# Performance work log

Measured on AMD Instinct MI355X. Metric: run time of the kernel, lower is better.

The kernel has to match this reference:

```python
import jax, jax.numpy as jnp
import numpy as np

N = 50000
E = 800000
HIDDEN = 128
NUM_HEADS = 8
D_HEAD = HIDDEN // NUM_HEADS


def setup_inputs() -> dict:
    key = jax.random.key(0)
    ks = jax.random.split(key, 12)
    sc = 1.0 / np.sqrt(HIDDEN)
    inp = {
        "h": jax.random.normal(ks[0], (N, HIDDEN), dtype=jnp.float32),
        "rows": jax.random.randint(ks[1], (E,), 0, N, dtype=jnp.int32),
        "cols": jax.random.randint(ks[2], (E,), 0, N, dtype=jnp.int32),
        "Wq": jax.random.normal(ks[3], (HIDDEN, HIDDEN), dtype=jnp.float32) * sc,
        "bq": jax.random.normal(ks[4], (HIDDEN,), dtype=jnp.float32) * sc,
        "Wk": jax.random.normal(ks[5], (HIDDEN, HIDDEN), dtype=jnp.float32) * sc,
        "bk": jax.random.normal(ks[6], (HIDDEN,), dtype=jnp.float32) * sc,
        "Wv": jax.random.normal(ks[7], (HIDDEN, HIDDEN), dtype=jnp.float32) * sc,
        "bv": jax.random.normal(ks[8], (HIDDEN,), dtype=jnp.float32) * sc,
        "Wo": jax.random.normal(ks[9], (HIDDEN, HIDDEN), dtype=jnp.float32) * sc,
        "bo": jax.random.normal(ks[10], (HIDDEN,), dtype=jnp.float32) * sc,
    }
    return inp


def reference(h, rows, cols, Wq, bq, Wk, bk, Wv, bv, Wo, bo):
    n = h.shape[0]
    scaling = D_HEAD ** (-0.5)
    # projections; torch-style reshape splits hidden as (d_head, num_heads)
    q = ((h @ Wq.T + bq).reshape(n, D_HEAD, NUM_HEADS)) * scaling
    k = (h @ Wk.T + bk).reshape(n, D_HEAD, NUM_HEADS)
    v = (h @ Wv.T + bv).reshape(n, D_HEAD, NUM_HEADS)
    # SDDMM: per-edge, per-head score = q[row] . k[col]   -> [E, H]
    scores = jnp.einsum("edh,edh->eh", q[rows], k[cols])
    # row-wise (destination) stable softmax over variable-degree neighborhoods
    m = jax.ops.segment_max(scores, rows, num_segments=n)  # [N, H]
    e = jnp.exp(scores - m[rows])
    s = jax.ops.segment_sum(e, rows, num_segments=n)  # [N, H]
    attn = e / s[rows]  # [E, H]
    # SpMM: out[i] = sum_{(i,j) in E} attn[e] * v[j]
    out = jax.ops.segment_sum(attn[:, None, :] * v[cols], rows, num_segments=n)
    return out.reshape(n, HIDDEN) @ Wo.T + bo
```

## Files before the change

kernel.cpp:

```cpp
#include <hip/hip_runtime.h>
#include <math.h>

#define N_NODES 50000
#define N_EDGES 800000
#define HID 128
#define CAP 64

#define SCAT_TH   (N_EDGES / 8)
#define SCAT_BLK  ((SCAT_TH + 255) / 256)
#define WCVT_BLK  64
#define HCVT_BLK  (N_NODES * HID / 4 / 256)
#define PREP_BLK  (SCAT_BLK + WCVT_BLK + HCVT_BLK)

#define QKV_BX    ((N_NODES + 31) / 32)
#define ATTN_BLK  ((N_NODES + 3) / 4)
#define OUT_BLK   ((N_NODES + 63) / 64)

typedef _Float16 f16_t;
typedef f16_t f16x8 __attribute__((ext_vector_type(8)));
typedef f16_t f16x2 __attribute__((ext_vector_type(2)));
typedef float f32x4 __attribute__((ext_vector_type(4)));

__device__ __forceinline__ ushort f2h_bits(float x) {
    union { f16_t h; ushort u; } c; c.h = (f16_t)x; return c.u;
}
__device__ __forceinline__ f16x2 as_h2(uint u) {
    union { uint u_; f16x2 h; } c; c.u_ = u; return c.h;
}

__global__ __launch_bounds__(256) void prep(
    const float* __restrict__ h,
    const float* __restrict__ Wq, const float* __restrict__ Wk,
    const float* __restrict__ Wv, const float* __restrict__ Wo,
    ushort* __restrict__ hf, ushort* __restrict__ wf,
    const int* __restrict__ rows, const int* __restrict__ cols,
    int* __restrict__ cnt, ushort* __restrict__ slots)
{
    const int b = blockIdx.x;
    const int tid = threadIdx.x;

    if (b < SCAT_BLK) {
        const int t = b * 256 + tid;
        if (t < SCAT_TH) {
            const int4* r4 = (const int4*)rows + (size_t)t * 2;
            const int4* c4 = (const int4*)cols + (size_t)t * 2;
            int4 ra = r4[0], rb2 = r4[1];
            int4 ca = c4[0], cb = c4[1];
            const int r[8] = {ra.x, ra.y, ra.z, ra.w, rb2.x, rb2.y, rb2.z, rb2.w};
            const int c[8] = {ca.x, ca.y, ca.z, ca.w, cb.x, cb.y, cb.z, cb.w};
            int p[8];
#pragma unroll
            for (int u = 0; u < 8; ++u)
                p[u] = atomicAdd(&cnt[r[u] << 4], 1);
#pragma unroll
            for (int u = 0; u < 8; ++u)
                if (p[u] < CAP) slots[(size_t)r[u] * CAP + p[u]] = (ushort)c[u];
        }
    } else if (b < SCAT_BLK + WCVT_BLK) {
        const int t = (b - SCAT_BLK) * 256 + tid;
        const int m = t >> 12, i = t & 4095;
        const float* src = (m == 0) ? Wq : (m == 1) ? Wk : (m == 2) ? Wv : Wo;
        float4 f = ((const float4*)src)[i];
        if (m < 3) {
            ushort4 o;
            o.x = f2h_bits(f.x); o.y = f2h_bits(f.y);
            o.z = f2h_bits(f.z); o.w = f2h_bits(f.w);
            ((ushort4*)(wf + m * 16384))[i] = o;
        } else {
            const int c  = i >> 5;
            const int k0 = (i & 31) * 4;
            const int d  = k0 >> 3;
            ushort* wo = wf + 3 * 16384 + c * HID + d;
            wo[((k0 + 0) & 7) << 4] = f2h_bits(f.x);
            wo[((k0 + 1) & 7) << 4] = f2h_bits(f.y);
            wo[((k0 + 2) & 7) << 4] = f2h_bits(f.z);
            wo[((k0 + 3) & 7) << 4] = f2h_bits(f.w);
        }
    } else {
        const int t = (b - SCAT_BLK - WCVT_BLK) * 256 + tid;
        float4 f = ((const float4*)h)[t];
        ushort4 o;
        o.x = f2h_bits(f.x); o.y = f2h_bits(f.y);
        o.z = f2h_bits(f.z); o.w = f2h_bits(f.w);
        ((ushort4*)hf)[t] = o;
    }
}

__global__ __launch_bounds__(256) void gemm_qkv(
    const ushort* __restrict__ hf, const ushort* __restrict__ wf,
    const float* __restrict__ bq, const float* __restrict__ bk,
    const float* __restrict__ bv,
    uint* __restrict__ qp, uint2* __restrict__ kv)
{
    const int lane = threadIdx.x & 63;
    const int wid  = threadIdx.x >> 6;
    const int mrow = lane & 15;
    const int quad = lane >> 4;
    const int rb   = blockIdx.x * 32;
    const int T    = blockIdx.y * 4 + wid;
    const int c    = ((mrow & 7) << 4) + ((mrow >> 3) << 3) + T;

    f16x8 a[2][4];
#pragma unroll
    for (int s = 0; s < 2; ++s) {
        int ar = rb + s * 16 + mrow;
        if (ar >= N_NODES) ar = N_NODES - 1;
        const ushort* ap = hf + (size_t)ar * HID + quad * 8;
#pragma unroll
        for (int kc = 0; kc < 4; ++kc) a[s][kc] = *(const f16x8*)(ap + kc * 32);
    }
    f16x8 bQ[4], bK[4], bV[4];
#pragma unroll
    for (int kc = 0; kc < 4; ++kc) {
        const int off = c * HID + kc * 32 + quad * 8;
        bQ[kc] = *(const f16x8*)(wf + off);
        bK[kc] = *(const f16x8*)(wf + 16384 + off);
        bV[kc] = *(const f16x8*)(wf + 32768 + off);
    }

    f32x4 aq[2], ak[2], av[2];
#pragma unroll
    for (int s = 0; s < 2; ++s) {
        aq[s] = (f32x4){0.f, 0.f, 0.f, 0.f};
        ak[s] = (f32x4){0.f, 0.f, 0.f, 0.f};
        av[s] = (f32x4){0.f, 0.f, 0.f, 0.f};
    }
#pragma unroll
    for (int s = 0; s < 2; ++s)
#pragma unroll
        for (int kc = 0; kc < 4; ++kc) {
            aq[s] = __builtin_amdgcn_mfma_f32_16x16x32_f16(a[s][kc], bQ[kc], aq[s], 0, 0, 0);
            ak[s] = __builtin_amdgcn_mfma_f32_16x16x32_f16(a[s][kc], bK[kc], ak[s], 0, 0, 0);
            av[s] = __builtin_amdgcn_mfma_f32_16x16x32_f16(a[s][kc], bV[kc], av[s], 0, 0, 0);
        }

    const float bqc = bq[c], bkc = bk[c], bvc = bv[c];
    const bool  lo  = (mrow & 8) == 0;
    const int   i   = mrow & 7;
#pragma unroll
    for (int s = 0; s < 2; ++s)
#pragma unroll
        for (int r = 0; r < 4; ++r) {
            const int orow = rb + s * 16 + quad * 4 + r;
            uint qv = f2h_bits((aq[s][r] + bqc) * 0.25f);
            uint kb = f2h_bits(ak[s][r] + bkc);
            uint vb = f2h_bits(av[s][r] + bvc);
            uint qh = __shfl_xor((int)qv, 8);
            uint kh = __shfl_xor((int)kb, 8);
            uint vh = __shfl_xor((int)vb, 8);
            if (lo && orow < N_NODES) {
                const size_t base = (size_t)orow * 64 + 8 * T + i;
                qp[base] = qv | (qh << 16);
                kv[base] = make_uint2(kb | (kh << 16), vb | (vh << 16));
            }
        }
}

__device__ __forceinline__ void pair_acc(uint4 rr, uint2 qu,
                                         float& l, float* O)
{
    float p = __builtin_amdgcn_fdot2(as_h2(rr.x), as_h2(qu.x), 0.f, false);
    p = __builtin_amdgcn_fdot2(as_h2(rr.z), as_h2(qu.y), p, false);
    p += __shfl_xor(p, 1);
    p += __shfl_xor(p, 2);
    const float ex = __expf(p);
    l += ex;
    const f16x2 va = as_h2(rr.y), vb = as_h2(rr.w);
    O[0] += ex * (float)va[0];
    O[1] += ex * (float)va[1];
    O[2] += ex * (float)vb[0];
    O[3] += ex * (float)vb[1];
}

__device__ __forceinline__ void pair_acc_m(uint4 rr, uint2 qu, bool ok,
                                           float& l, float* O)
{
    float p = __builtin_amdgcn_fdot2(as_h2(rr.x), as_h2(qu.x), 0.f, false);
    p = __builtin_amdgcn_fdot2(as_h2(rr.z), as_h2(qu.y), p, false);
    p += __shfl_xor(p, 1);
    p += __shfl_xor(p, 2);
    const float ex = ok ? __expf(p) : 0.f;
    l += ex;
    const f16x2 va = as_h2(rr.y), vb = as_h2(rr.w);
    O[0] += ex * (float)va[0];
    O[1] += ex * (float)va[1];
    O[2] += ex * (float)vb[0];
    O[3] += ex * (float)vb[1];
}

__global__ __launch_bounds__(256) void attn(
    const uint* __restrict__ qp, const uint2* __restrict__ kv,
    const int* __restrict__ cnt, const ushort* __restrict__ slots,
    ushort* __restrict__ ao)
{
    const int lane = threadIdx.x & 63;
    const int node = blockIdx.x * 4 + (threadIdx.x >> 6);
    if (node >= N_NODES) return;
    const int half = lane >> 5;
    const int t    = lane & 31;

    const uint2 qu = *(const uint2*)(qp + (size_t)node * 64 + 2 * t);

    int deg = cnt[node << 4];
    if (deg > CAP) deg = CAP;
    const int myslot = (lane < deg) ? (int)slots[(size_t)node * CAP + lane] : 0;

    float l0 = 0.f, l1 = 0.f, l2 = 0.f, l3 = 0.f;
    float O0[4] = {0,0,0,0}, O1[4] = {0,0,0,0};
    float O2[4] = {0,0,0,0}, O3[4] = {0,0,0,0};

    const uint4* base = (const uint4*)kv;

    int j = 0;
    for (; j + 8 <= deg; j += 8) {
        const int s0 = __shfl(myslot, j + half);
        const int s1 = __shfl(myslot, j + 2 + half);
        const int s2 = __shfl(myslot, j + 4 + half);
        const int s3 = __shfl(myslot, j + 6 + half);
        const uint4 r0 = base[(size_t)s0 * 32 + t];
        const uint4 r1 = base[(size_t)s1 * 32 + t];
        const uint4 r2 = base[(size_t)s2 * 32 + t];
        const uint4 r3 = base[(size_t)s3 * 32 + t];
        pair_acc(r0, qu, l0, O0);
        pair_acc(r1, qu, l1, O1);
        pair_acc(r2, qu, l2, O2);
        pair_acc(r3, qu, l3, O3);
    }
    for (; j < deg; j += 2) {
        const int e = j + half;
        const int s = __shfl(myslot, e);
        const uint4 rr = base[(size_t)s * 32 + t];
        pair_acc_m(rr, qu, e < deg, l0, O0);
    }

    float l = (l0 + l1) + (l2 + l3);
    float Of[4];
    Of[0] = (O0[0] + O1[0]) + (O2[0] + O3[0]);
    Of[1] = (O0[1] + O1[1]) + (O2[1] + O3[1]);
    Of[2] = (O0[2] + O1[2]) + (O2[2] + O3[2]);
    Of[3] = (O0[3] + O1[3]) + (O2[3] + O3[3]);

    l += __shfl_xor(l, 32);
    Of[0] += __shfl_xor(Of[0], 32);
    Of[1] += __shfl_xor(Of[1], 32);
    Of[2] += __shfl_xor(Of[2], 32);
    Of[3] += __shfl_xor(Of[3], 32);

    const float inv = (l > 0.f) ? 1.f / l : 0.f;

    if (half == 0) {
        ushort4 st;
        st.x = f2h_bits(Of[0] * inv);
        st.y = f2h_bits(Of[1] * inv);
        st.z = f2h_bits(Of[2] * inv);
        st.w = f2h_bits(Of[3] * inv);
        *(ushort4*)(ao + (size_t)node * HID + 4 * t) = st;
    }
}

__global__ __launch_bounds__(256) void gemm_out(
    const ushort* __restrict__ A, const ushort* __restrict__ wfo,
    const float* __restrict__ bias, float* __restrict__ out)
{
    const int lane = threadIdx.x & 63;
    const int wid  = threadIdx.x >> 6;
    const int mrow = lane & 15;
    const int quad = lane >> 4;
    const int rb   = blockIdx.x * 64;

    const int c0 = wid * 32 + mrow;
    const int c1 = c0 + 16;

    f16x8 a[4][4];
#pragma unroll
    for (int s = 0; s < 4; ++s) {
        int ar = rb + s * 16 + mrow;
        if (ar >= N_NODES) ar = N_NODES - 1;
        const ushort* ap = A + (size_t)ar * HID + quad * 8;
#pragma unroll
        for (int kc = 0; kc < 4; ++kc) a[s][kc] = *(const f16x8*)(ap + kc * 32);
    }
    f16x8 b0[4], b1[4];
#pragma unroll
    for (int kc = 0; kc < 4; ++kc) {
        b0[kc] = *(const f16x8*)(wfo + c0 * HID + kc * 32 + quad * 8);
        b1[kc] = *(const f16x8*)(wfo + c1 * HID + kc * 32 + quad * 8);
    }

    f32x4 acc[4][2];
#pragma unroll
    for (int s = 0; s < 4; ++s) {
        acc[s][0] = (f32x4){0.f, 0.f, 0.f, 0.f};
        acc[s][1] = (f32x4){0.f, 0.f, 0.f, 0.f};
    }
#pragma unroll
    for (int s = 0; s < 4; ++s)
#pragma unroll
        for (int kc = 0; kc < 4; ++kc) {
            acc[s][0] = __builtin_amdgcn_mfma_f32_16x16x32_f16(a[s][kc], b0[kc], acc[s][0], 0, 0, 0);
            acc[s][1] = __builtin_amdgcn_mfma_f32_16x16x32_f16(a[s][kc], b1[kc], acc[s][1], 0, 0, 0);
        }

    const float bc0 = bias[c0], bc1 = bias[c1];
#pragma unroll
    for (int s = 0; s < 4; ++s)
#pragma unroll
        for (int r = 0; r < 4; ++r) {
            const int orow = rb + s * 16 + quad * 4 + r;
            if (orow < N_NODES) {
                out[(size_t)orow * HID + c0] = acc[s][0][r] + bc0;
                out[(size_t)orow * HID + c1] = acc[s][1][r] + bc1;
            }
        }
}

extern "C" void kernel_launch(void* const* d_in, const int* in_sizes, int n_in,
                              void* d_out, int out_size, void* d_ws, size_t ws_size,
                              hipStream_t stream)
{
    const float* h    = (const float*)d_in[0];
    const int*   rows = (const int*)  d_in[1];
    const int*   cols = (const int*)  d_in[2];
    const float* Wq   = (const float*)d_in[3];
    const float* bq   = (const float*)d_in[4];
    const float* Wk   = (const float*)d_in[5];
    const float* bk   = (const float*)d_in[6];
    const float* Wv   = (const float*)d_in[7];
    const float* bv   = (const float*)d_in[8];
    const float* Wo   = (const float*)d_in[9];
    const float* bo   = (const float*)d_in[10];
    float* out = (float*)d_out;

    char* ws = (char*)d_ws;
    uint*   qp    = (uint*)ws;    ws += (size_t)N_NODES * 64 * 4;
    uint2*  kv    = (uint2*)ws;   ws += (size_t)N_NODES * 64 * 8;
    ushort* hf    = (ushort*)ws;  ws += (size_t)N_NODES * HID * 2;
    ushort* ao    = (ushort*)ws;  ws += (size_t)N_NODES * HID * 2;
    ushort* wf    = (ushort*)ws;  ws += 4 * 16384 * 2;
    int*    cnt   = (int*)ws;     ws += (size_t)N_NODES * 64;
    ushort* slots = (ushort*)ws;

    hipMemsetAsync(cnt, 0, (size_t)N_NODES * 64, stream);

    dim3 blk(256);
    prep<<<PREP_BLK, blk, 0, stream>>>(h, Wq, Wk, Wv, Wo, hf, wf,
                                       rows, cols, cnt, slots);
    gemm_qkv<<<dim3(QKV_BX, 2), blk, 0, stream>>>(hf, wf, bq, bk, bv, qp, kv);
    attn<<<ATTN_BLK, blk, 0, stream>>>(qp, kv, cnt, slots, ao);
    gemm_out<<<OUT_BLK, blk, 0, stream>>>(ao, wf + 3 * 16384, bo, out);
}
```

Before: 238.4 us.

## Fuse fp32-to-fp16 conversion and edge scatter into the QKV GEMM launch

Removes the separate prep pass that converted h and Wq/Wk/Wv to fp16. The QKV GEMM blocks now read fp32 h and weights directly and convert in registers. The edge scatter and Wo conversion blocks share the same launch. This drops the hf round trip through memory (a write and a re-read of N×128 halves) and one kernel launch, at the cost of reading fp32 inputs, which doubles the bytes for the A operand, and converting the weights redundantly in every block.

```diff
diff --git a/kernel.cpp b/kernel.cpp
--- a/kernel.cpp
+++ b/kernel.cpp
@@ -8,11 +8,11 @@
 
 #define SCAT_TH   (N_EDGES / 8)
 #define SCAT_BLK  ((SCAT_TH + 255) / 256)
-#define WCVT_BLK  64
-#define HCVT_BLK  (N_NODES * HID / 4 / 256)
-#define PREP_BLK  (SCAT_BLK + WCVT_BLK + HCVT_BLK)
-
+#define WOCVT_BLK 16
 #define QKV_BX    ((N_NODES + 31) / 32)
+#define QKV_BLKS  (QKV_BX * 2)
+#define FUSED1_BLK (SCAT_BLK + WOCVT_BLK + QKV_BLKS)
+
 #define ATTN_BLK  ((N_NODES + 3) / 4)
 #define OUT_BLK   ((N_NODES + 63) / 64)
 
@@ -27,14 +27,25 @@
 __device__ __forceinline__ f16x2 as_h2(uint u) {
     union { uint u_; f16x2 h; } c; c.u_ = u; return c.h;
 }
-
-__global__ __launch_bounds__(256) void prep(
+__device__ __forceinline__ f16x8 ldcvt8(const float* __restrict__ p) {
+    float4 f0 = *(const float4*)p;
+    float4 f1 = *(const float4*)(p + 4);
+    f16x8 r;
+    r[0] = (f16_t)f0.x; r[1] = (f16_t)f0.y; r[2] = (f16_t)f0.z; r[3] = (f16_t)f0.w;
+    r[4] = (f16_t)f1.x; r[5] = (f16_t)f1.y; r[6] = (f16_t)f1.z; r[7] = (f16_t)f1.w;
+    return r;
+}
+
+__global__ __launch_bounds__(256) void fused1(
     const float* __restrict__ h,
     const float* __restrict__ Wq, const float* __restrict__ Wk,
     const float* __restrict__ Wv, const float* __restrict__ Wo,
-    ushort* __restrict__ hf, ushort* __restrict__ wf,
+    const float* __restrict__ bq, const float* __restrict__ bk,
+    const float* __restrict__ bv,
     const int* __restrict__ rows, const int* __restrict__ cols,
-    int* __restrict__ cnt, ushort* __restrict__ slots)
+    int* __restrict__ cnt, ushort* __restrict__ slots,
+    ushort* __restrict__ wfo,
+    uint* __restrict__ qp, uint2* __restrict__ kv)
 {
     const int b = blockIdx.x;
     const int tid = threadIdx.x;
@@ -56,48 +67,31 @@
             for (int u = 0; u < 8; ++u)
                 if (p[u] < CAP) slots[(size_t)r[u] * CAP + p[u]] = (ushort)c[u];
         }
-    } else if (b < SCAT_BLK + WCVT_BLK) {
-        const int t = (b - SCAT_BLK) * 256 + tid;
-        const int m = t >> 12, i = t & 4095;
-        const float* src = (m == 0) ? Wq : (m == 1) ? Wk : (m == 2) ? Wv : Wo;
-        float4 f = ((const float4*)src)[i];
-        if (m < 3) {
-            ushort4 o;
-            o.x = f2h_bits(f.x); o.y = f2h_bits(f.y);
-            o.z = f2h_bits(f.z); o.w = f2h_bits(f.w);
-            ((ushort4*)(wf + m * 16384))[i] = o;
-        } else {
-            const int c  = i >> 5;
-            const int k0 = (i & 31) * 4;
-            const int d  = k0 >> 3;
-            ushort* wo = wf + 3 * 16384 + c * HID + d;
-            wo[((k0 + 0) & 7) << 4] = f2h_bits(f.x);
-            wo[((k0 + 1) & 7) << 4] = f2h_bits(f.y);
-            wo[((k0 + 2) & 7) << 4] = f2h_bits(f.z);
-            wo[((k0 + 3) & 7) << 4] = f2h_bits(f.w);
-        }
-    } else {
-        const int t = (b - SCAT_BLK - WCVT_BLK) * 256 + tid;
-        float4 f = ((const float4*)h)[t];
-        ushort4 o;
-        o.x = f2h_bits(f.x); o.y = f2h_bits(f.y);
-        o.z = f2h_bits(f.z); o.w = f2h_bits(f.w);
-        ((ushort4*)hf)[t] = o;
-    }
-}
-
-__global__ __launch_bounds__(256) void gemm_qkv(
-    const ushort* __restrict__ hf, const ushort* __restrict__ wf,
-    const float* __restrict__ bq, const float* __restrict__ bk,
-    const float* __restrict__ bv,
-    uint* __restrict__ qp, uint2* __restrict__ kv)
-{
-    const int lane = threadIdx.x & 63;
-    const int wid  = threadIdx.x >> 6;
+        return;
+    }
+    if (b < SCAT_BLK + WOCVT_BLK) {
+        const int i = (b - SCAT_BLK) * 256 + tid;
+        float4 f = ((const float4*)Wo)[i];
+        const int c  = i >> 5;
+        const int k0 = (i & 31) * 4;
+        const int d  = k0 >> 3;
+        ushort* wo = wfo + c * HID + d;
+        wo[((k0 + 0) & 7) << 4] = f2h_bits(f.x);
+        wo[((k0 + 1) & 7) << 4] = f2h_bits(f.y);
+        wo[((k0 + 2) & 7) << 4] = f2h_bits(f.z);
+        wo[((k0 + 3) & 7) << 4] = f2h_bits(f.w);
+        return;
+    }
+
+    const int qb   = b - (SCAT_BLK + WOCVT_BLK);
+    const int by   = (qb >= QKV_BX) ? 1 : 0;
+    const int bx   = qb - by * QKV_BX;
+    const int lane = tid & 63;
+    const int wid  = tid >> 6;
     const int mrow = lane & 15;
     const int quad = lane >> 4;
-    const int rb   = blockIdx.x * 32;
-    const int T    = blockIdx.y * 4 + wid;
+    const int rb   = bx * 32;
+    const int T    = by * 4 + wid;
     const int c    = ((mrow & 7) << 4) + ((mrow >> 3) << 3) + T;
 
     f16x8 a[2][4];
@@ -105,17 +99,17 @@
     for (int s = 0; s < 2; ++s) {
         int ar = rb + s * 16 + mrow;
         if (ar >= N_NODES) ar = N_NODES - 1;
-        const ushort* ap = hf + (size_t)ar * HID + quad * 8;
-#pragma unroll
-        for (int kc = 0; kc < 4; ++kc) a[s][kc] = *(const f16x8*)(ap + kc * 32);
+        const float* ap = h + (size_t)ar * HID + quad * 8;
+#pragma unroll
+        for (int kc = 0; kc < 4; ++kc) a[s][kc] = ldcvt8(ap + kc * 32);
     }
     f16x8 bQ[4], bK[4], bV[4];
 #pragma unroll
     for (int kc = 0; kc < 4; ++kc) {
         const int off = c * HID + kc * 32 + quad * 8;
-        bQ[kc] = *(const f16x8*)(wf + off);
-        bK[kc] = *(const f16x8*)(wf + 16384 + off);
-        bV[kc] = *(const f16x8*)(wf + 32768 + off);
+        bQ[kc] = ldcvt8(Wq + off);
+        bK[kc] = ldcvt8(Wk + off);
+        bV[kc] = ldcvt8(Wv + off);
     }
 
     f32x4 aq[2], ak[2], av[2];
@@ -334,18 +328,16 @@
     char* ws = (char*)d_ws;
     uint*   qp    = (uint*)ws;    ws += (size_t)N_NODES * 64 * 4;
     uint2*  kv    = (uint2*)ws;   ws += (size_t)N_NODES * 64 * 8;
-    ushort* hf    = (ushort*)ws;  ws += (size_t)N_NODES * HID * 2;
     ushort* ao    = (ushort*)ws;  ws += (size_t)N_NODES * HID * 2;
-    ushort* wf    = (ushort*)ws;  ws += 4 * 16384 * 2;
+    ushort* wfo   = (ushort*)ws;  ws += 16384 * 2;
     int*    cnt   = (int*)ws;     ws += (size_t)N_NODES * 64;
     ushort* slots = (ushort*)ws;
 
     hipMemsetAsync(cnt, 0, (size_t)N_NODES * 64, stream);
 
     dim3 blk(256);
-    prep<<<PREP_BLK, blk, 0, stream>>>(h, Wq, Wk, Wv, Wo, hf, wf,
-                                       rows, cols, cnt, slots);
-    gemm_qkv<<<dim3(QKV_BX, 2), blk, 0, stream>>>(hf, wf, bq, bk, bv, qp, kv);
+    fused1<<<FUSED1_BLK, blk, 0, stream>>>(h, Wq, Wk, Wv, Wo, bq, bk, bv,
+                                           rows, cols, cnt, slots, wfo, qp, kv);
     attn<<<ATTN_BLK, blk, 0, stream>>>(qp, kv, cnt, slots, ao);
-    gemm_out<<<OUT_BLK, blk, 0, stream>>>(ao, wf + 3 * 16384, bo, out);
-}
+    gemm_out<<<OUT_BLK, blk, 0, stream>>>(ao, wfo, bo, out);
+}
```

Measured after the change: 252.9 us. +6.1%, slower.

## Fuse attention aggregation with output projection via shared memory tile

Applied to the files above, without the earlier changes.

Merges the attention kernel and the output GEMM into one kernel. Each 512-thread block aggregates 64 nodes into an LDS tile and then runs the MFMA projection from LDS, so the fp16 intermediate no longer goes through global memory. The QKV GEMM also goes from a 2-D grid of 256-thread blocks to 1-D blocks of 512 threads, which covers all column tiles per block and reuses the A fragment. The price is that each wave now processes 8 nodes serially, a block barrier stalls on the slowest wave's degree, and the larger blocks may lower occupancy for the gather-heavy phase.

```diff
diff --git a/kernel.cpp b/kernel.cpp
--- a/kernel.cpp
+++ b/kernel.cpp
@@ -13,8 +13,7 @@
 #define PREP_BLK  (SCAT_BLK + WCVT_BLK + HCVT_BLK)
 
 #define QKV_BX    ((N_NODES + 31) / 32)
-#define ATTN_BLK  ((N_NODES + 3) / 4)
-#define OUT_BLK   ((N_NODES + 63) / 64)
+#define AO_BLK    ((N_NODES + 63) / 64)
 
 typedef _Float16 f16_t;
 typedef f16_t f16x8 __attribute__((ext_vector_type(8)));
@@ -86,18 +85,18 @@
     }
 }
 
-__global__ __launch_bounds__(256) void gemm_qkv(
+__global__ __launch_bounds__(512) void gemm_qkv(
     const ushort* __restrict__ hf, const ushort* __restrict__ wf,
     const float* __restrict__ bq, const float* __restrict__ bk,
     const float* __restrict__ bv,
     uint* __restrict__ qp, uint2* __restrict__ kv)
 {
-    const int lane = threadIdx.x & 63;
-    const int wid  = threadIdx.x >> 6;
+    const int tid  = threadIdx.x;
+    const int lane = tid & 63;
+    const int T    = tid >> 6;
     const int mrow = lane & 15;
     const int quad = lane >> 4;
     const int rb   = blockIdx.x * 32;
-    const int T    = blockIdx.y * 4 + wid;
     const int c    = ((mrow & 7) << 4) + ((mrow >> 3) << 3) + T;
 
     f16x8 a[2][4];
@@ -188,129 +187,123 @@
     O[3] += ex * (float)vb[1];
 }
 
-__global__ __launch_bounds__(256) void attn(
+#define ALS_STRIDE 136
+
+__global__ __launch_bounds__(512) void attn_out(
     const uint* __restrict__ qp, const uint2* __restrict__ kv,
     const int* __restrict__ cnt, const ushort* __restrict__ slots,
-    ushort* __restrict__ ao)
-{
-    const int lane = threadIdx.x & 63;
-    const int node = blockIdx.x * 4 + (threadIdx.x >> 6);
-    if (node >= N_NODES) return;
+    const ushort* __restrict__ wfo, const float* __restrict__ bo,
+    float* __restrict__ out)
+{
+    __shared__ ushort als[64][ALS_STRIDE];
+
+    const int tid  = threadIdx.x;
+    const int lane = tid & 63;
+    const int w    = tid >> 6;
+    const int rb   = blockIdx.x * 64;
     const int half = lane >> 5;
     const int t    = lane & 31;
 
-    const uint2 qu = *(const uint2*)(qp + (size_t)node * 64 + 2 * t);
-
-    int deg = cnt[node << 4];
-    if (deg > CAP) deg = CAP;
-    const int myslot = (lane < deg) ? (int)slots[(size_t)node * CAP + lane] : 0;
-
-    float l0 = 0.f, l1 = 0.f, l2 = 0.f, l3 = 0.f;
-    float O0[4] = {0,0,0,0}, O1[4] = {0,0,0,0};
-    float O2[4] = {0,0,0,0}, O3[4] = {0,0,0,0};
-
     const uint4* base = (const uint4*)kv;
 
-    int j = 0;
-    for (; j + 8 <= deg; j += 8) {
-        const int s0 = __shfl(myslot, j + half);
-        const int s1 = __shfl(myslot, j + 2 + half);
-        const int s2 = __shfl(myslot, j + 4 + half);
-        const int s3 = __shfl(myslot, j + 6 + half);
-        const uint4 r0 = base[(size_t)s0 * 32 + t];
-        const uint4 r1 = base[(size_t)s1 * 32 + t];
-        const uint4 r2 = base[(size_t)s2 * 32 + t];
-        const uint4 r3 = base[(size_t)s3 * 32 + t];
-        pair_acc(r0, qu, l0, O0);
-        pair_acc(r1, qu, l1, O1);
-        pair_acc(r2, qu, l2, O2);
-        pair_acc(r3, qu, l3, O3);
-    }
-    for (; j < deg; j += 2) {
-        const int e = j + half;
-        const int s = __shfl(myslot, e);
-        const uint4 rr = base[(size_t)s * 32 + t];
-        pair_acc_m(rr, qu, e < deg, l0, O0);
-    }
-
-    float l = (l0 + l1) + (l2 + l3);
-    float Of[4];
-    Of[0] = (O0[0] + O1[0]) + (O2[0] + O3[0]);
-    Of[1] = (O0[1] + O1[1]) + (O2[1] + O3[1]);
-    Of[2] = (O0[2] + O1[2]) + (O2[2] + O3[2]);
-    Of[3] = (O0[3] + O1[3]) + (O2[3] + O3[3]);
-
-    l += __shfl_xor(l, 32);
-    Of[0] += __shfl_xor(Of[0], 32);
-    Of[1] += __shfl_xor(Of[1], 32);
-    Of[2] += __shfl_xor(Of[2], 32);
-    Of[3] += __shfl_xor(Of[3], 32);
-
-    const float inv = (l > 0.f) ? 1.f / l : 0.f;
-
-    if (half == 0) {
-        ushort4 st;
-        st.x = f2h_bits(Of[0] * inv);
-        st.y = f2h_bits(Of[1] * inv);
-        st.z = f2h_bits(Of[2] * inv);
-        st.w = f2h_bits(Of[3] * inv);
-        *(ushort4*)(ao + (size_t)node * HID + 4 * t) = st;
-    }
-}
-
-__global__ __launch_bounds__(256) void gemm_out(
-    const ushort* __restrict__ A, const ushort* __restrict__ wfo,
-    const float* __restrict__ bias, float* __restrict__ out)
-{
-    const int lane = threadIdx.x & 63;
-    const int wid  = threadIdx.x >> 6;
+    for (int it = 0; it < 8; ++it) {
+        const int local = w * 8 + it;
+        const int node  = rb + local;
+        if (node < N_NODES) {
+            const uint2 qu = *(const uint2*)(qp + (size_t)node * 64 + 2 * t);
+
+            int deg = cnt[node << 4];
+            if (deg > CAP) deg = CAP;
+            const int myslot = (lane < deg) ? (int)slots[(size_t)node * CAP + lane] : 0;
+
+            float l0 = 0.f, l1 = 0.f, l2 = 0.f, l3 = 0.f;
+            float O0[4] = {0,0,0,0}, O1[4] = {0,0,0,0};
+            float O2[4] = {0,0,0,0}, O3[4] = {0,0,0,0};
+
+            int j = 0;
+            for (; j + 8 <= deg; j += 8) {
+                const int s0 = __shfl(myslot, j + half);
+                const int s1 = __shfl(myslot, j + 2 + half);
+                const int s2 = __shfl(myslot, j + 4 + half);
+                const int s3 = __shfl(myslot, j + 6 + half);
+                const uint4 r0 = base[(size_t)s0 * 32 + t];
+                const uint4 r1 = base[(size_t)s1 * 32 + t];
+                const uint4 r2 = base[(size_t)s2 * 32 + t];
+                const uint4 r3 = base[(size_t)s3 * 32 + t];
+                pair_acc(r0, qu, l0, O0);
+                pair_acc(r1, qu, l1, O1);
+                pair_acc(r2, qu, l2, O2);
+                pair_acc(r3, qu, l3, O3);
+            }
+            for (; j < deg; j += 2) {
+                const int e = j + half;
+                const int s = __shfl(myslot, e);
+                const uint4 rr = base[(size_t)s * 32 + t];
+                pair_acc_m(rr, qu, e < deg, l0, O0);
+            }
+
+            float l = (l0 + l1) + (l2 + l3);
+            float Of[4];
+            Of[0] = (O0[0] + O1[0]) + (O2[0] + O3[0]);
+            Of[1] = (O0[1] + O1[1]) + (O2[1] + O3[1]);
+            Of[2] = (O0[2] + O1[2]) + (O2[2] + O3[2]);
+            Of[3] = (O0[3] + O1[3]) + (O2[3] + O3[3]);
+
+            l += __shfl_xor(l, 32);
+            Of[0] += __shfl_xor(Of[0], 32);
+            Of[1] += __shfl_xor(Of[1], 32);
+            Of[2] += __shfl_xor(Of[2], 32);
+            Of[3] += __shfl_xor(Of[3], 32);
+
+            const float inv = (l > 0.f) ? 1.f / l : 0.f;
+
+            if (half == 0) {
+                ushort4 st;
+                st.x = f2h_bits(Of[0] * inv);
+                st.y = f2h_bits(Of[1] * inv);
+                st.z = f2h_bits(Of[2] * inv);
+                st.w = f2h_bits(Of[3] * inv);
+                *(ushort4*)&als[local][4 * t] = st;
+            }
+        } else if (half == 0) {
+            *(ushort4*)&als[local][4 * t] = (ushort4){0, 0, 0, 0};
+        }
+    }
+
+    __syncthreads();
+
     const int mrow = lane & 15;
     const int quad = lane >> 4;
-    const int rb   = blockIdx.x * 64;
-
-    const int c0 = wid * 32 + mrow;
-    const int c1 = c0 + 16;
-
-    f16x8 a[4][4];
+    const int c    = w * 16 + mrow;
+
+    f16x8 bfr[4];
+#pragma unroll
+    for (int kc = 0; kc < 4; ++kc)
+        bfr[kc] = *(const f16x8*)(wfo + c * HID + kc * 32 + quad * 8);
+
+    f32x4 acc[4];
+#pragma unroll
+    for (int s = 0; s < 4; ++s) acc[s] = (f32x4){0.f, 0.f, 0.f, 0.f};
+
 #pragma unroll
     for (int s = 0; s < 4; ++s) {
-        int ar = rb + s * 16 + mrow;
-        if (ar >= N_NODES) ar = N_NODES - 1;
-        const ushort* ap = A + (size_t)ar * HID + quad * 8;
-#pragma unroll
-        for (int kc = 0; kc < 4; ++kc) a[s][kc] = *(const f16x8*)(ap + kc * 32);
-    }
-    f16x8 b0[4], b1[4];
-#pragma unroll
-    for (int kc = 0; kc < 4; ++kc) {
-        b0[kc] = *(const f16x8*)(wfo + c0 * HID + kc * 32 + quad * 8);
-        b1[kc] = *(const f16x8*)(wfo + c1 * HID + kc * 32 + quad * 8);
-    }
-
-    f32x4 acc[4][2];
-#pragma unroll
-    for (int s = 0; s < 4; ++s) {
-        acc[s][0] = (f32x4){0.f, 0.f, 0.f, 0.f};
-        acc[s][1] = (f32x4){0.f, 0.f, 0.f, 0.f};
-    }
-#pragma unroll
-    for (int s = 0; s < 4; ++s)
-#pragma unroll
-        for (int kc = 0; kc < 4; ++kc) {
-            acc[s][0] = __builtin_amdgcn_mfma_f32_16x16x32_f16(a[s][kc], b0[kc], acc[s][0], 0, 0, 0);
-            acc[s][1] = __builtin_amdgcn_mfma_f32_16x16x32_f16(a[s][kc], b1[kc], acc[s][1], 0, 0, 0);
-        }
-
-    const float bc0 = bias[c0], bc1 = bias[c1];
+        f16x8 afr[4];
+#pragma unroll
+        for (int kc = 0; kc < 4; ++kc)
+            afr[kc] = *(const f16x8*)&als[s * 16 + mrow][quad * 8 + kc * 32];
+#pragma unroll
+        for (int kc = 0; kc < 4; ++kc)
+            acc[s] = __builtin_amdgcn_mfma_f32_16x16x32_f16(afr[kc], bfr[kc], acc[s], 0, 0, 0);
+    }
+
+    const float bc = bo[c];
 #pragma unroll
     for (int s = 0; s < 4; ++s)
 #pragma unroll
         for (int r = 0; r < 4; ++r) {
             const int orow = rb + s * 16 + quad * 4 + r;
-            if (orow < N_NODES) {
-                out[(size_t)orow * HID + c0] = acc[s][0][r] + bc0;
-                out[(size_t)orow * HID + c1] = acc[s][1][r] + bc1;
-            }
+            if (orow < N_NODES)
+                out[(size_t)orow * HID + c] = acc[s][r] + bc;
         }
 }
 
@@ -335,17 +328,15 @@
     uint*   qp    = (uint*)ws;    ws += (size_t)N_NODES * 64 * 4;
     uint2*  kv    = (uint2*)ws;   ws += (size_t)N_NODES * 64 * 8;
     ushort* hf    = (ushort*)ws;  ws += (size_t)N_NODES * HID * 2;
-    ushort* ao    = (ushort*)ws;  ws += (size_t)N_NODES * HID * 2;
     ushort* wf    = (ushort*)ws;  ws += 4 * 16384 * 2;
     int*    cnt   = (int*)ws;     ws += (size_t)N_NODES * 64;
     ushort* slots = (ushort*)ws;
 
     hipMemsetAsync(cnt, 0, (size_t)N_NODES * 64, stream);
 
-    dim3 blk(256);
-    prep<<<PREP_BLK, blk, 0, stream>>>(h, Wq, Wk, Wv, Wo, hf, wf,
-                                       rows, cols, cnt, slots);
-    gemm_qkv<<<dim3(QKV_BX, 2), blk, 0, stream>>>(hf, wf, bq, bk, bv, qp, kv);
-    attn<<<ATTN_BLK, blk, 0, stream>>>(qp, kv, cnt, slots, ao);
-    gemm_out<<<OUT_BLK, blk, 0, stream>>>(ao, wf + 3 * 16384, bo, out);
-}
+    prep<<<PREP_BLK, dim3(256), 0, stream>>>(h, Wq, Wk, Wv, Wo, hf, wf,
+                                             rows, cols, cnt, slots);
+    gemm_qkv<<<QKV_BX, dim3(512), 0, stream>>>(hf, wf, bq, bk, bv, qp, kv);
+    attn_out<<<AO_BLK, dim3(512), 0, stream>>>(qp, kv, cnt, slots,
+                                               wf + 3 * 16384, bo, out);
+}
```

Measured after the change: 251.1 us. +5.3%, slower.

## Stage QKV GEMM outputs in LDS for coalesced full-row stores

Applied to the files above, without the earlier changes.

The QKV projection kernel now runs 8 waves per 512-thread block, so one block covers all 64 output columns of its 32 rows and the second grid dimension is dropped. Each wave's packed q and kv results go into padded shared-memory tiles. After a barrier the block writes whole contiguous rows with 16-byte stores, replacing the scattered 4- and 8-byte global writes. This costs extra LDS capacity and a block-wide barrier, and the larger block may reduce occupancy.

```diff
diff --git a/kernel.cpp b/kernel.cpp
--- a/kernel.cpp
+++ b/kernel.cpp
@@ -86,18 +86,24 @@
     }
 }
 
-__global__ __launch_bounds__(256) void gemm_qkv(
+#define QLS_STRIDE 66
+#define KLS_STRIDE 65
+
+__global__ __launch_bounds__(512) void gemm_qkv(
     const ushort* __restrict__ hf, const ushort* __restrict__ wf,
     const float* __restrict__ bq, const float* __restrict__ bk,
     const float* __restrict__ bv,
     uint* __restrict__ qp, uint2* __restrict__ kv)
 {
-    const int lane = threadIdx.x & 63;
-    const int wid  = threadIdx.x >> 6;
+    __shared__ uint  qls[32 * QLS_STRIDE];
+    __shared__ uint2 kls[32 * KLS_STRIDE];
+
+    const int tid  = threadIdx.x;
+    const int lane = tid & 63;
+    const int T    = tid >> 6;
     const int mrow = lane & 15;
     const int quad = lane >> 4;
     const int rb   = blockIdx.x * 32;
-    const int T    = blockIdx.y * 4 + wid;
     const int c    = ((mrow & 7) << 4) + ((mrow >> 3) << 3) + T;
 
     f16x8 a[2][4];
@@ -141,19 +147,39 @@
     for (int s = 0; s < 2; ++s)
 #pragma unroll
         for (int r = 0; r < 4; ++r) {
-            const int orow = rb + s * 16 + quad * 4 + r;
+            const int lrow = s * 16 + quad * 4 + r;
             uint qv = f2h_bits((aq[s][r] + bqc) * 0.25f);
             uint kb = f2h_bits(ak[s][r] + bkc);
             uint vb = f2h_bits(av[s][r] + bvc);
             uint qh = __shfl_xor((int)qv, 8);
             uint kh = __shfl_xor((int)kb, 8);
             uint vh = __shfl_xor((int)vb, 8);
-            if (lo && orow < N_NODES) {
-                const size_t base = (size_t)orow * 64 + 8 * T + i;
-                qp[base] = qv | (qh << 16);
-                kv[base] = make_uint2(kb | (kh << 16), vb | (vh << 16));
+            if (lo) {
+                qls[lrow * QLS_STRIDE + 8 * T + i] = qv | (qh << 16);
+                kls[lrow * KLS_STRIDE + 8 * T + i] = make_uint2(kb | (kh << 16), vb | (vh << 16));
             }
         }
+
+    __syncthreads();
+
+    {
+        const int row = tid >> 4;
+        if (rb + row < N_NODES) {
+            const int col4 = (tid & 15) * 4;
+            uint4 v = *(const uint4*)&qls[row * QLS_STRIDE + col4];
+            ((uint4*)(qp + (size_t)rb * 64))[tid] = v;
+        }
+    }
+#pragma unroll
+    for (int k = 0; k < 2; ++k) {
+        const int u   = tid + k * 512;
+        const int row = u >> 5;
+        if (rb + row < N_NODES) {
+            const int q4 = u & 31;
+            uint4 v = *(const uint4*)&kls[row * KLS_STRIDE + q4 * 2];
+            ((uint4*)(kv + (size_t)rb * 64))[u] = v;
+        }
+    }
 }
 
 __device__ __forceinline__ void pair_acc(uint4 rr, uint2 qu,
@@ -342,10 +368,9 @@
 
     hipMemsetAsync(cnt, 0, (size_t)N_NODES * 64, stream);
 
-    dim3 blk(256);
-    prep<<<PREP_BLK, blk, 0, stream>>>(h, Wq, Wk, Wv, Wo, hf, wf,
-                                       rows, cols, cnt, slots);
-    gemm_qkv<<<dim3(QKV_BX, 2), blk, 0, stream>>>(hf, wf, bq, bk, bv, qp, kv);
-    attn<<<ATTN_BLK, blk, 0, stream>>>(qp, kv, cnt, slots, ao);
-    gemm_out<<<OUT_BLK, blk, 0, stream>>>(ao, wf + 3 * 16384, bo, out);
-}
+    prep<<<PREP_BLK, dim3(256), 0, stream>>>(h, Wq, Wk, Wv, Wo, hf, wf,
+                                             rows, cols, cnt, slots);
+    gemm_qkv<<<QKV_BX, dim3(512), 0, stream>>>(hf, wf, bq, bk, bv, qp, kv);
+    attn<<<ATTN_BLK, dim3(256), 0, stream>>>(qp, kv, cnt, slots, ao);
+    gemm_out<<<OUT_BLK, dim3(256), 0, stream>>>(ao, wf + 3 * 16384, bo, out);
+}
```

After: 240.3 us. Within noise of the previous version (+0.8%).
